# Kernel optimization log

Hardware: AMD Instinct MI355X
Metric: run time of the kernel (lower is better)

Reference implementation:

```python
import jax, jax.numpy as jnp
import numpy as np

# Model dims (match init_kwargs)
H = 1024            # hidden_size
I = 2048            # intermediate_size (per expert)
NH = 16             # num_heads
HD = H // NH        # head_dim = 64
E = 8               # num_experts
TOPK = 2
MAX_SEQ = 2048
EPS = 1e-6
NEG = -1e9


def precompute_freqs_cis(dim, max_seq_len, theta=10000.0):
    # Faithful to source: cat([cos, sin], dim=-1) -> shape [S, dim]
    pos = np.arange(max_seq_len, dtype=np.float32)
    freqs = np.arange(0, dim, 2, dtype=np.float32) / dim
    inv_freq = 1.0 / (theta ** freqs)
    f = np.einsum('i,j->ij', pos, inv_freq)
    return jnp.asarray(np.concatenate([np.cos(f), np.sin(f)], axis=-1), dtype=jnp.float32)


def setup_inputs() -> dict:
    key = jax.random.key(0)
    ks = jax.random.split(key, 12)
    B, S = 2, 1024
    s = lambda fan: 1.0 / np.sqrt(fan)
    inp = {
        'x': jax.random.normal(ks[0], (B, S, H), dtype=jnp.float32),
        'attn_norm_w': jnp.ones((H,), dtype=jnp.float32),
        'ffn_norm_w': jnp.ones((H,), dtype=jnp.float32),
        'wq': jax.random.normal(ks[1], (H, H), dtype=jnp.float32) * s(H),
        'wk': jax.random.normal(ks[2], (H, H), dtype=jnp.float32) * s(H),
        'wv': jax.random.normal(ks[3], (H, H), dtype=jnp.float32) * s(H),
        'wo': jax.random.normal(ks[4], (H, H), dtype=jnp.float32) * s(H),
        'router_w': jax.random.normal(ks[5], (H, E), dtype=jnp.float32) * s(H),
        'w1': jax.random.normal(ks[6], (E, H, I), dtype=jnp.float32) * s(H),
        'w3': jax.random.normal(ks[7], (E, H, I), dtype=jnp.float32) * s(H),
        'w2': jax.random.normal(ks[8], (E, I, H), dtype=jnp.float32) * s(I),
        'freqs_cis': precompute_freqs_cis(HD, MAX_SEQ),
    }
    return inp


def rmsnorm(x, w):
    rms = jnp.sqrt(jnp.mean(x * x, axis=-1, keepdims=True) + EPS)
    return w * (x / rms)


def apply_rope(x, freqs_cis):
    # x: [B, S, NH, HD]; faithful to source pairing (interleaved view of cat(cos,sin))
    B, S, nh, hd = x.shape
    xr = x.reshape(B, S, nh, hd // 2, 2)
    fr = freqs_cis[:S].reshape(1, S, 1, hd // 2, 2)  # position_ids = arange(S)
    a, b = xr[..., 0], xr[..., 1]
    cr, ci = fr[..., 0], fr[..., 1]
    out = jnp.stack([a * cr - b * ci, a * ci + b * cr], axis=-1)
    return out.reshape(B, S, nh, hd)


def attention(x, wq, wk, wv, wo, freqs_cis):
    B, S, _ = x.shape
    q = (x @ wq).reshape(B, S, NH, HD)
    k = (x @ wk).reshape(B, S, NH, HD)
    v = (x @ wv).reshape(B, S, NH, HD)
    q = apply_rope(q, freqs_cis)
    k = apply_rope(k, freqs_cis)
    # [B, NH, S, S]
    scores = jnp.einsum('bqhd,bkhd->bhqk', q, k) / np.sqrt(HD).astype(np.float32)
    causal = jnp.tril(jnp.ones((S, S), dtype=bool))
    scores = jnp.where(causal[None, None], scores, NEG)
    attn = jax.nn.softmax(scores, axis=-1)
    out = jnp.einsum('bhqk,bkhd->bqhd', attn, v).reshape(B, S, H)
    return out @ wo


def moe_ffn(x, router_w, w1, w2, w3):
    # x: [B, S, H] -> flatten tokens
    B, S, _ = x.shape
    xt = x.reshape(B * S, H)                      # [T, H]
    logits = xt @ router_w                        # [T, E]
    probs = jax.nn.softmax(logits, axis=-1)
    topv, topi = jax.lax.top_k(probs, TOPK)       # [T, K]
    topv = topv / jnp.sum(topv, axis=-1, keepdims=True)  # renormalize top-k weights
    # combine[t, e] = sum_k topv[t,k] * 1[topi[t,k]==e]
    combine = jnp.sum(topv[..., None] * jax.nn.one_hot(topi, E, dtype=xt.dtype), axis=1)  # [T, E]
    # SwiGLU experts, dense over experts (mathematically identical to no-drop routing)
    h1 = jnp.einsum('th,ehi->eti', xt, w1)
    h3 = jnp.einsum('th,ehi->eti', xt, w3)
    ye = jnp.einsum('eti,eih->eth', jax.nn.silu(h1) * h3, w2)  # [E, T, H]
    out = jnp.einsum('te,eth->th', combine, ye)
    return out.reshape(B, S, H)


def reference(x, attn_norm_w, ffn_norm_w, wq, wk, wv, wo, router_w, w1, w3, w2, freqs_cis):
    h = x + attention(rmsnorm(x, attn_norm_w), wq, wk, wv, wo, freqs_cis)
    out = h + moe_ffn(rmsnorm(h, ffn_norm_w), router_w, w1, w2, w3)
    return out
```

## Files before the change

### kernel.cpp

```cpp
#include <hip/hip_runtime.h>
#include <hip/hip_bf16.h>
#include <math.h>

#define HS 1024
#define IS 2048
#define NHEAD 16
#define HDIM 64
#define NEXP 8
#define BATCH 2
#define SEQ 1024
#define NTOK (BATCH*SEQ)
#define NASSIGN (NTOK*2)
#define QKVW 3072
#define PAD 72
#define MAXBLK 40

typedef short bf16x8 __attribute__((ext_vector_type(8)));
typedef float f32x4  __attribute__((ext_vector_type(4)));

__device__ __forceinline__ void ldsdma16(void* lds, const void* gp) {
    __builtin_amdgcn_global_load_lds(
        (const __attribute__((address_space(1))) void*)gp,
        (__attribute__((address_space(3))) void*)lds, 16, 0, 0);
}

__global__ void rmsnorm_split(const float* __restrict__ x, const float* __restrict__ w,
                              __hip_bfloat16* __restrict__ oh, __hip_bfloat16* __restrict__ ol) {
    int t = blockIdx.x;
    int tid = threadIdx.x;
    const float* row = x + (size_t)t * HS;
    float ss = 0.f;
    for (int i = tid; i < HS; i += 256) { float v = row[i]; ss += v * v; }
    for (int off = 32; off > 0; off >>= 1) ss += __shfl_down(ss, off);
    __shared__ float red[4];
    if ((tid & 63) == 0) red[tid >> 6] = ss;
    __syncthreads();
    float tot = red[0] + red[1] + red[2] + red[3];
    float rr = rsqrtf(tot / (float)HS + 1e-6f);
    for (int i = tid; i < HS; i += 256) {
        float v = w[i] * row[i] * rr;
        __hip_bfloat16 hi = __float2bfloat16(v);
        oh[(size_t)t * HS + i] = hi;
        ol[(size_t)t * HS + i] = __float2bfloat16(v - __bfloat162float(hi));
    }
}

__global__ void rmsnorm_dual(const float* __restrict__ x, const float* __restrict__ w,
                             float* __restrict__ outf, __hip_bfloat16* __restrict__ outb) {
    int t = blockIdx.x;
    int tid = threadIdx.x;
    const float* row = x + (size_t)t * HS;
    float ss = 0.f;
    for (int i = tid; i < HS; i += 256) { float v = row[i]; ss += v * v; }
    for (int off = 32; off > 0; off >>= 1) ss += __shfl_down(ss, off);
    __shared__ float red[4];
    if ((tid & 63) == 0) red[tid >> 6] = ss;
    __syncthreads();
    float tot = red[0] + red[1] + red[2] + red[3];
    float rr = rsqrtf(tot / (float)HS + 1e-6f);
    for (int i = tid; i < HS; i += 256) {
        float v = w[i] * row[i] * rr;
        outf[(size_t)t * HS + i] = v;
        outb[(size_t)t * HS + i] = __float2bfloat16(v);
    }
}

__global__ void transpose_split(const float* __restrict__ src,
                                __hip_bfloat16* __restrict__ dh, __hip_bfloat16* __restrict__ dl,
                                int R, int C, int rowOff) {
    __shared__ float tile[32][33];
    int c0 = blockIdx.x * 32, r0 = blockIdx.y * 32;
    int tx = threadIdx.x & 31, ty = threadIdx.x >> 5;
    #pragma unroll
    for (int i = 0; i < 4; i++) {
        int r = ty + i * 8;
        tile[r][tx] = src[(size_t)(r0 + r) * C + c0 + tx];
    }
    __syncthreads();
    #pragma unroll
    for (int i = 0; i < 4; i++) {
        int c = ty + i * 8;
        float v = tile[tx][c];
        __hip_bfloat16 hi = __float2bfloat16(v);
        size_t o = (size_t)(rowOff + c0 + c) * R + r0 + tx;
        dh[o] = hi;
        dl[o] = __float2bfloat16(v - __bfloat162float(hi));
    }
}

__global__ void transpose_bf16(const float* __restrict__ in, __hip_bfloat16* __restrict__ outp,
                               int R, int C) {
    __shared__ float tile[32][33];
    int e = blockIdx.z;
    const float* src = in + (size_t)e * R * C;
    __hip_bfloat16* dst = outp + (size_t)e * R * C;
    int c0 = blockIdx.x * 32, r0 = blockIdx.y * 32;
    int tx = threadIdx.x & 31, ty = threadIdx.x >> 5;
    #pragma unroll
    for (int i = 0; i < 4; i++) {
        int r = ty + i * 8;
        tile[r][tx] = src[(size_t)(r0 + r) * C + c0 + tx];
    }
    __syncthreads();
    #pragma unroll
    for (int i = 0; i < 4; i++) {
        int c = ty + i * 8;
        dst[(size_t)(c0 + c) * R + r0 + tx] = __float2bfloat16(tile[tx][c]);
    }
}

__global__ __launch_bounds__(256) void gemm_bf16x3(const __hip_bfloat16* __restrict__ Ah,
                                                   const __hip_bfloat16* __restrict__ Al,
                                                   const __hip_bfloat16* __restrict__ Bh,
                                                   const __hip_bfloat16* __restrict__ Bl,
                                                   const float* __restrict__ resid,
                                                   float* __restrict__ C,
                                                   int M, int N, int K) {
    __shared__ __align__(16) short Ahs[128][32];
    __shared__ __align__(16) short Als[128][32];
    __shared__ __align__(16) short Bhs[128][32];
    __shared__ __align__(16) short Bls[128][32];
    int bm = blockIdx.y * 128, bn = blockIdx.x * 128;
    int t = threadIdx.x;
    int wave = t >> 6, lane = t & 63;
    int wm = (wave & 1) * 64, wn = (wave >> 1) * 64;
    int fr = lane & 15, quad = lane >> 4;
    int r0 = wave * 32;
    int srow = lane >> 2;
    int schunk = (lane & 3) ^ ((lane >> 3) & 3);
    const __hip_bfloat16* pAh0 = Ah + (size_t)(bm + r0 + srow) * K + schunk * 8;
    const __hip_bfloat16* pAh1 = pAh0 + (size_t)16 * K;
    const __hip_bfloat16* pAl0 = Al + (size_t)(bm + r0 + srow) * K + schunk * 8;
    const __hip_bfloat16* pAl1 = pAl0 + (size_t)16 * K;
    const __hip_bfloat16* pBh0 = Bh + (size_t)(bn + r0 + srow) * K + schunk * 8;
    const __hip_bfloat16* pBh1 = pBh0 + (size_t)16 * K;
    const __hip_bfloat16* pBl0 = Bl + (size_t)(bn + r0 + srow) * K + schunk * 8;
    const __hip_bfloat16* pBl1 = pBl0 + (size_t)16 * K;
    int ca = (quad ^ ((fr >> 1) & 3)) * 8;

    f32x4 acc[4][4] = {};
    for (int k0 = 0; k0 < K; k0 += 32) {
        ldsdma16(&Ahs[r0][0],      pAh0 + k0);
        ldsdma16(&Ahs[r0 + 16][0], pAh1 + k0);
        ldsdma16(&Als[r0][0],      pAl0 + k0);
        ldsdma16(&Als[r0 + 16][0], pAl1 + k0);
        ldsdma16(&Bhs[r0][0],      pBh0 + k0);
        ldsdma16(&Bhs[r0 + 16][0], pBh1 + k0);
        ldsdma16(&Bls[r0][0],      pBl0 + k0);
        ldsdma16(&Bls[r0 + 16][0], pBl1 + k0);
        __syncthreads();
        bf16x8 ah[4], bh[4], x[4];
        #pragma unroll
        for (int i = 0; i < 4; i++) {
            ah[i] = *(const bf16x8*)&Ahs[wm + i * 16 + fr][ca];
            bh[i] = *(const bf16x8*)&Bhs[wn + i * 16 + fr][ca];
        }
        #pragma unroll
        for (int mi = 0; mi < 4; mi++)
            #pragma unroll
            for (int ni = 0; ni < 4; ni++)
                acc[mi][ni] = __builtin_amdgcn_mfma_f32_16x16x32_bf16(ah[mi], bh[ni], acc[mi][ni], 0, 0, 0);
        #pragma unroll
        for (int i = 0; i < 4; i++) x[i] = *(const bf16x8*)&Bls[wn + i * 16 + fr][ca];
        #pragma unroll
        for (int mi = 0; mi < 4; mi++)
            #pragma unroll
            for (int ni = 0; ni < 4; ni++)
                acc[mi][ni] = __builtin_amdgcn_mfma_f32_16x16x32_bf16(ah[mi], x[ni], acc[mi][ni], 0, 0, 0);
        #pragma unroll
        for (int i = 0; i < 4; i++) x[i] = *(const bf16x8*)&Als[wm + i * 16 + fr][ca];
        #pragma unroll
        for (int mi = 0; mi < 4; mi++)
            #pragma unroll
            for (int ni = 0; ni < 4; ni++)
                acc[mi][ni] = __builtin_amdgcn_mfma_f32_16x16x32_bf16(x[mi], bh[ni], acc[mi][ni], 0, 0, 0);
        __syncthreads();
    }
    int rq = quad * 4;
    #pragma unroll
    for (int mi = 0; mi < 4; mi++) {
        #pragma unroll
        for (int r = 0; r < 4; r++) {
            size_t rowo = (size_t)(bm + wm + mi * 16 + rq + r) * N + bn + wn;
            #pragma unroll
            for (int ni = 0; ni < 4; ni++) {
                float v = acc[mi][ni][r];
                size_t o = rowo + ni * 16 + fr;
                if (resid) v += resid[o];
                C[o] = v;
            }
        }
    }
}

__global__ void rope_convert(const float* __restrict__ qkv, const float* __restrict__ fc,
                             __hip_bfloat16* __restrict__ qh, __hip_bfloat16* __restrict__ ql,
                             __hip_bfloat16* __restrict__ kh, __hip_bfloat16* __restrict__ kl,
                             __hip_bfloat16* __restrict__ vh, __hip_bfloat16* __restrict__ vl) {
    int t = blockIdx.x;
    int s = t & (SEQ - 1);
    const float* row = qkv + (size_t)t * QKVW;
    size_t ob = (size_t)t * HS;
    for (int p = threadIdx.x; p < 512; p += 256) {
        int hh = p >> 5, j = p & 31;
        int col = hh * 64 + 2 * j;
        float cr = fc[s * HDIM + 2 * j];
        float ci = fc[s * HDIM + 2 * j + 1];
        float a = row[col], b = row[col + 1];
        float r0 = a * cr - b * ci, r1 = a * ci + b * cr;
        __hip_bfloat16 h0 = __float2bfloat16(r0), h1 = __float2bfloat16(r1);
        qh[ob + col] = h0;     ql[ob + col]     = __float2bfloat16(r0 - __bfloat162float(h0));
        qh[ob + col + 1] = h1; ql[ob + col + 1] = __float2bfloat16(r1 - __bfloat162float(h1));
        a = row[1024 + col]; b = row[1024 + col + 1];
        r0 = a * cr - b * ci; r1 = a * ci + b * cr;
        h0 = __float2bfloat16(r0); h1 = __float2bfloat16(r1);
        kh[ob + col] = h0;     kl[ob + col]     = __float2bfloat16(r0 - __bfloat162float(h0));
        kh[ob + col + 1] = h1; kl[ob + col + 1] = __float2bfloat16(r1 - __bfloat162float(h1));
        r0 = row[2048 + col]; r1 = row[2048 + col + 1];
        h0 = __float2bfloat16(r0); h1 = __float2bfloat16(r1);
        vh[ob + col] = h0;     vl[ob + col]     = __float2bfloat16(r0 - __bfloat162float(h0));
        vh[ob + col + 1] = h1; vl[ob + col + 1] = __float2bfloat16(r1 - __bfloat162float(h1));
    }
}

__global__ __launch_bounds__(256) void attn_partial(
        const __hip_bfloat16* __restrict__ qh, const __hip_bfloat16* __restrict__ ql,
        const __hip_bfloat16* __restrict__ kh, const __hip_bfloat16* __restrict__ kl,
        const __hip_bfloat16* __restrict__ vh, const __hip_bfloat16* __restrict__ vl,
        float* __restrict__ po, float* __restrict__ pm_g, float* __restrict__ pl_g) {
    int c = blockIdx.x, qt = blockIdx.y;
    int nc = (qt + 4) >> 2;
    if (c >= nc) return;
    int bh = blockIdx.z;
    int b = bh >> 4, h = bh & 15;
    int t0 = c * 4, t1 = min(t0 + 4, qt + 1);
    int tid = threadIdx.x;
    int wave = tid >> 6, lane = tid & 63;
    int fr = lane & 15, quad = lane >> 4;
    int w16 = wave * 16;
    __shared__ __align__(16) short Qh[64][PAD], Ql[64][PAD];
    __shared__ __align__(16) short KPh[64][PAD], KPl[64][PAD];
    __shared__ __align__(16) short Vhs[64][PAD], Vls[64][PAD];
    size_t hoff = (size_t)h * HDIM;
    int sr = tid >> 2, sg = tid & 3;
    {
        const __hip_bfloat16* qp  = qh + (size_t)(b * SEQ + qt * 64 + sr) * HS + hoff;
        const __hip_bfloat16* qp2 = ql + (size_t)(b * SEQ + qt * 64 + sr) * HS + hoff;
        *(uint4*)&Qh[sr][sg * 8]       = *(const uint4*)(qp + sg * 8);
        *(uint4*)&Qh[sr][(sg + 4) * 8] = *(const uint4*)(qp + (sg + 4) * 8);
        *(uint4*)&Ql[sr][sg * 8]       = *(const uint4*)(qp2 + sg * 8);
        *(uint4*)&Ql[sr][(sg + 4) * 8] = *(const uint4*)(qp2 + (sg + 4) * 8);
    }
    f32x4 o[4] = {};
    float mrow[4], lrow[4];
    #pragma unroll
    for (int i = 0; i < 4; i++) { mrow[i] = -1e30f; lrow[i] = 0.f; }
    int key0 = (tid & 31) * 2, ds = tid >> 5;
    __syncthreads();

    for (int kt = t0; kt < t1; kt++) {
        int kbase = kt * 64;
        {
            const __hip_bfloat16* kp  = kh + (size_t)(b * SEQ + kbase + sr) * HS + hoff;
            const __hip_bfloat16* kp2 = kl + (size_t)(b * SEQ + kbase + sr) * HS + hoff;
            *(uint4*)&KPh[sr][sg * 8]       = *(const uint4*)(kp + sg * 8);
            *(uint4*)&KPh[sr][(sg + 4) * 8] = *(const uint4*)(kp + (sg + 4) * 8);
            *(uint4*)&KPl[sr][sg * 8]       = *(const uint4*)(kp2 + sg * 8);
            *(uint4*)&KPl[sr][(sg + 4) * 8] = *(const uint4*)(kp2 + (sg + 4) * 8);
        }
        {
            const __hip_bfloat16* v0 = vh + (size_t)(b * SEQ + kbase + key0) * HS + hoff + ds * 8;
            uint4 A = *(const uint4*)v0;
            uint4 Bv = *(const uint4*)(v0 + HS);
            const unsigned short* ap = (const unsigned short*)&A;
            const unsigned short* bp = (const unsigned short*)&Bv;
            #pragma unroll
            for (int j = 0; j < 8; j++)
                *(unsigned*)&Vhs[ds * 8 + j][key0] = (unsigned)ap[j] | ((unsigned)bp[j] << 16);
            const __hip_bfloat16* v2 = vl + (size_t)(b * SEQ + kbase + key0) * HS + hoff + ds * 8;
            uint4 A2 = *(const uint4*)v2;
            uint4 B2 = *(const uint4*)(v2 + HS);
            const unsigned short* ap2 = (const unsigned short*)&A2;
            const unsigned short* bp2 = (const unsigned short*)&B2;
            #pragma unroll
            for (int j = 0; j < 8; j++)
                *(unsigned*)&Vls[ds * 8 + j][key0] = (unsigned)ap2[j] | ((unsigned)bp2[j] << 16);
        }
        __syncthreads();

        f32x4 s[4] = {};
        #pragma unroll
        for (int ks = 0; ks < 2; ks++) {
            bf16x8 a_h = *(const bf16x8*)&Qh[w16 + fr][quad * 8 + ks * 32];
            bf16x8 a_l = *(const bf16x8*)&Ql[w16 + fr][quad * 8 + ks * 32];
            #pragma unroll
            for (int ni = 0; ni < 4; ni++) {
                bf16x8 b_h = *(const bf16x8*)&KPh[ni * 16 + fr][quad * 8 + ks * 32];
                bf16x8 b_l = *(const bf16x8*)&KPl[ni * 16 + fr][quad * 8 + ks * 32];
                s[ni] = __builtin_amdgcn_mfma_f32_16x16x32_bf16(a_h, b_h, s[ni], 0, 0, 0);
                s[ni] = __builtin_amdgcn_mfma_f32_16x16x32_bf16(a_h, b_l, s[ni], 0, 0, 0);
                s[ni] = __builtin_amdgcn_mfma_f32_16x16x32_bf16(a_l, b_h, s[ni], 0, 0, 0);
            }
        }
        int qg = qt * 64 + w16 + quad * 4;
        #pragma unroll
        for (int ni = 0; ni < 4; ni++) {
            int kg = kbase + ni * 16 + fr;
            #pragma unroll
            for (int r = 0; r < 4; r++)
                s[ni][r] = (kg > qg + r) ? -1e9f : s[ni][r] * 0.125f;
        }
        #pragma unroll
        for (int r = 0; r < 4; r++) {
            float mx = fmaxf(fmaxf(s[0][r], s[1][r]), fmaxf(s[2][r], s[3][r]));
            #pragma unroll
            for (int wd = 1; wd < 16; wd <<= 1) mx = fmaxf(mx, __shfl_xor(mx, wd));
            float nm = fmaxf(mrow[r], mx);
            float alpha = __expf(mrow[r] - nm);
            float rs = 0.f;
            #pragma unroll
            for (int ni = 0; ni < 4; ni++) { float e = __expf(s[ni][r] - nm); s[ni][r] = e; rs += e; }
            #pragma unroll
            for (int wd = 1; wd < 16; wd <<= 1) rs += __shfl_xor(rs, wd);
            lrow[r] = lrow[r] * alpha + rs;
            mrow[r] = nm;
            o[0][r] *= alpha; o[1][r] *= alpha; o[2][r] *= alpha; o[3][r] *= alpha;
        }
        __syncthreads();
        #pragma unroll
        for (int ni = 0; ni < 4; ni++)
            #pragma unroll
            for (int r = 0; r < 4; r++) {
                float pv = s[ni][r];
                __hip_bfloat16 hi = __float2bfloat16(pv);
                __hip_bfloat16 lo = __float2bfloat16(pv - __bfloat162float(hi));
                KPh[w16 + quad * 4 + r][ni * 16 + fr] = *(short*)&hi;
                KPl[w16 + quad * 4 + r][ni * 16 + fr] = *(short*)&lo;
            }
        #pragma unroll
        for (int ks = 0; ks < 2; ks++) {
            bf16x8 p_h = *(const bf16x8*)&KPh[w16 + fr][quad * 8 + ks * 32];
            bf16x8 p_l = *(const bf16x8*)&KPl[w16 + fr][quad * 8 + ks * 32];
            #pragma unroll
            for (int ni = 0; ni < 4; ni++) {
                bf16x8 v_h = *(const bf16x8*)&Vhs[ni * 16 + fr][quad * 8 + ks * 32];
                bf16x8 v_l = *(const bf16x8*)&Vls[ni * 16 + fr][quad * 8 + ks * 32];
                o[ni] = __builtin_amdgcn_mfma_f32_16x16x32_bf16(p_h, v_h, o[ni], 0, 0, 0);
                o[ni] = __builtin_amdgcn_mfma_f32_16x16x32_bf16(p_h, v_l, o[ni], 0, 0, 0);
                o[ni] = __builtin_amdgcn_mfma_f32_16x16x32_bf16(p_l, v_h, o[ni], 0, 0, 0);
            }
        }
        __syncthreads();
    }
    int pidx = (bh * 16 + qt) * 4 + c;
    float* pob = po + (size_t)pidx * 4096;
    #pragma unroll
    for (int ni = 0; ni < 4; ni++)
        #pragma unroll
        for (int r = 0; r < 4; r++)
            pob[(w16 + quad * 4 + r) * 64 + ni * 16 + fr] = o[ni][r];
    if (fr == 0) {
        #pragma unroll
        for (int r = 0; r < 4; r++) {
            pm_g[pidx * 64 + w16 + quad * 4 + r] = mrow[r];
            pl_g[pidx * 64 + w16 + quad * 4 + r] = lrow[r];
        }
    }
}

__global__ void attn_merge(const float* __restrict__ po, const float* __restrict__ pm,
                           const float* __restrict__ pl,
                           __hip_bfloat16* __restrict__ ch, __hip_bfloat16* __restrict__ cl) {
    int qt = blockIdx.x, h = blockIdx.y, b = blockIdx.z;
    int bh = b * 16 + h;
    int nc = (qt + 4) >> 2;
    int base = (bh * 16 + qt) * 4;
    int tid = threadIdx.x;
    int r  = tid >> 2;
    int d0 = (tid & 3) * 16;
    float mstar = -1e30f;
    for (int c = 0; c < nc; c++) mstar = fmaxf(mstar, pm[(base + c) * 64 + r]);
    float a[4];
    float lsum = 0.f;
    for (int c = 0; c < nc; c++) {
        a[c] = __expf(pm[(base + c) * 64 + r] - mstar);
        lsum += a[c] * pl[(base + c) * 64 + r];
    }
    float inv = 1.f / lsum;
    size_t crow = (size_t)(b * SEQ + qt * 64 + r) * HS + h * HDIM;
    for (int dd = 0; dd < 16; dd += 4) {
        float4 acc = make_float4(0.f, 0.f, 0.f, 0.f);
        for (int c = 0; c < nc; c++) {
            float4 v = *(const float4*)(po + (size_t)(base + c) * 4096 + r * 64 + d0 + dd);
            acc.x += a[c] * v.x; acc.y += a[c] * v.y;
            acc.z += a[c] * v.z; acc.w += a[c] * v.w;
        }
        float vs[4] = {acc.x * inv, acc.y * inv, acc.z * inv, acc.w * inv};
        #pragma unroll
        for (int j = 0; j < 4; j++) {
            __hip_bfloat16 hi = __float2bfloat16(vs[j]);
            ch[crow + d0 + dd + j] = hi;
            cl[crow + d0 + dd + j] = __float2bfloat16(vs[j] - __bfloat162float(hi));
        }
    }
}

__global__ void router_kernel(const float* __restrict__ hn, const float* __restrict__ rw,
                              int* __restrict__ cnt, int* __restrict__ topEk,
                              float* __restrict__ topW) {
    int t = blockIdx.x;
    int lane = threadIdx.x;
    float acc[NEXP];
    #pragma unroll
    for (int e = 0; e < NEXP; e++) acc[e] = 0.f;
    const float* row = hn + (size_t)t * HS;
    for (int kk = lane; kk < HS; kk += 64) {
        float xv = row[kk];
        const float* r = rw + (size_t)kk * NEXP;
        #pragma unroll
        for (int e = 0; e < NEXP; e++) acc[e] += xv * r[e];
    }
    #pragma unroll
    for (int e = 0; e < NEXP; e++)
        for (int off = 32; off > 0; off >>= 1) acc[e] += __shfl_down(acc[e], off);
    if (lane == 0) {
        float mx = acc[0];
        #pragma unroll
        for (int e = 1; e < NEXP; e++) mx = fmaxf(mx, acc[e]);
        float p[NEXP]; float s = 0.f;
        #pragma unroll
        for (int e = 0; e < NEXP; e++) { p[e] = __expf(acc[e] - mx); s += p[e]; }
        int i0 = 0;
        #pragma unroll
        for (int e = 1; e < NEXP; e++) if (p[e] > p[i0]) i0 = e;
        int i1 = (i0 == 0) ? 1 : 0;
        #pragma unroll
        for (int e = 0; e < NEXP; e++) if (e != i0 && p[e] > p[i1]) i1 = e;
        float v0 = p[i0], v1 = p[i1], sn = v0 + v1;
        topEk[2 * t]     = i0; topW[2 * t]     = v0 / sn;
        topEk[2 * t + 1] = i1; topW[2 * t + 1] = v1 / sn;
        atomicAdd(&cnt[i0], 1);
        atomicAdd(&cnt[i1], 1);
    }
}

__global__ void offsets_kernel(const int* __restrict__ cnt, int* __restrict__ off,
                               int* __restrict__ blk_e, int* __restrict__ blk_r) {
    if (threadIdx.x == 0) {
        int o = 0, n = 0;
        for (int e = 0; e < NEXP; e++) {
            off[e] = o;
            for (int bm = 0; bm < cnt[e]; bm += 128) { blk_e[n] = e; blk_r[n] = bm; n++; }
            o += cnt[e];
        }
        for (; n < MAXBLK; n++) { blk_e[n] = -1; blk_r[n] = 0; }
    }
}

__global__ void scatter_kernel(const int* __restrict__ topEk, int* __restrict__ fill,
                               const int* __restrict__ off, const float* __restrict__ topW,
                               int* __restrict__ tok_list, float* __restrict__ wA) {
    int idx = blockIdx.x * 256 + threadIdx.x;
    int e = topEk[idx];
    int slot = atomicAdd(&fill[e], 1);
    int gidx = off[e] + slot;
    tok_list[gidx] = idx >> 1;
    wA[gidx] = topW[idx];
}

__global__ __launch_bounds__(256) void moe_up_mfma(const __hip_bfloat16* __restrict__ Abf,
                                                   const __hip_bfloat16* __restrict__ B1T,
                                                   const __hip_bfloat16* __restrict__ B3T,
                                                   __hip_bfloat16* __restrict__ g,
                                                   const int* __restrict__ cnt,
                                                   const int* __restrict__ off,
                                                   const int* __restrict__ tok_list,
                                                   const int* __restrict__ blk_e,
                                                   const int* __restrict__ blk_r) {
    int e = blk_e[blockIdx.y];
    if (e < 0) return;
    int bm = blk_r[blockIdx.y];
    int ce = cnt[e], oe = off[e];
    int bn = blockIdx.x * 128;
    const __hip_bfloat16* b1 = B1T + (size_t)e * IS * HS;
    const __hip_bfloat16* b3 = B3T + (size_t)e * IS * HS;

    __shared__ __align__(16) short As[128][32];
    __shared__ __align__(16) short B1s[128][32];
    __shared__ __align__(16) short B3s[128][32];

    int t = threadIdx.x;
    int wave = t >> 6, lane = t & 63;
    int wm = (wave & 1) * 64, wn = (wave >> 1) * 64;
    int fr = lane & 15, quad = lane >> 4;
    int r0 = wave * 32;
    int srow = lane >> 2;
    int schunk = (lane & 3) ^ ((lane >> 3) & 3);
    int tokA0 = tok_list[oe + min(bm + r0 + srow, ce - 1)];
    int tokA1 = tok_list[oe + min(bm + r0 + 16 + srow, ce - 1)];
    const __hip_bfloat16* pA0 = Abf + (size_t)tokA0 * HS + schunk * 8;
    const __hip_bfloat16* pA1 = Abf + (size_t)tokA1 * HS + schunk * 8;
    const __hip_bfloat16* pB1a = b1 + (size_t)(bn + r0 + srow) * HS + schunk * 8;
    const __hip_bfloat16* pB1b = pB1a + (size_t)16 * HS;
    const __hip_bfloat16* pB3a = b3 + (size_t)(bn + r0 + srow) * HS + schunk * 8;
    const __hip_bfloat16* pB3b = pB3a + (size_t)16 * HS;
    int ca = (quad ^ ((fr >> 1) & 3)) * 8;

    f32x4 acc1[4][4] = {};
    f32x4 acc3[4][4] = {};

    for (int k0 = 0; k0 < HS; k0 += 32) {
        ldsdma16(&As[r0][0],       pA0 + k0);
        ldsdma16(&As[r0 + 16][0],  pA1 + k0);
        ldsdma16(&B1s[r0][0],      pB1a + k0);
        ldsdma16(&B1s[r0 + 16][0], pB1b + k0);
        ldsdma16(&B3s[r0][0],      pB3a + k0);
        ldsdma16(&B3s[r0 + 16][0], pB3b + k0);
        __syncthreads();
        bf16x8 a[4], f1[4], f3[4];
        #pragma unroll
        for (int i = 0; i < 4; i++) {
            a[i]  = *(const bf16x8*)&As[wm + i * 16 + fr][ca];
            f1[i] = *(const bf16x8*)&B1s[wn + i * 16 + fr][ca];
            f3[i] = *(const bf16x8*)&B3s[wn + i * 16 + fr][ca];
        }
        #pragma unroll
        for (int mi = 0; mi < 4; mi++)
            #pragma unroll
            for (int ni = 0; ni < 4; ni++) {
                acc1[mi][ni] = __builtin_amdgcn_mfma_f32_16x16x32_bf16(a[mi], f1[ni], acc1[mi][ni], 0, 0, 0);
                acc3[mi][ni] = __builtin_amdgcn_mfma_f32_16x16x32_bf16(a[mi], f3[ni], acc3[mi][ni], 0, 0, 0);
            }
        __syncthreads();
    }
    int rq = quad * 4;
    #pragma unroll
    for (int mi = 0; mi < 4; mi++) {
        #pragma unroll
        for (int r = 0; r < 4; r++) {
            int slot = bm + wm + mi * 16 + rq + r;
            if (slot < ce) {
                size_t rowo = (size_t)(oe + slot) * IS + bn + wn;
                #pragma unroll
                for (int ni = 0; ni < 4; ni++) {
                    float x1 = acc1[mi][ni][r];
                    float x3 = acc3[mi][ni][r];
                    float sv = (x1 / (1.f + __expf(-x1))) * x3;
                    g[rowo + ni * 16 + fr] = __float2bfloat16(sv);
                }
            }
        }
    }
}

__global__ __launch_bounds__(256) void moe_down_mfma(const __hip_bfloat16* __restrict__ g,
                                                     const __hip_bfloat16* __restrict__ B2T,
                                                     float* __restrict__ out,
                                                     const int* __restrict__ cnt,
                                                     const int* __restrict__ off,
                                                     const int* __restrict__ tok_list,
                                                     const float* __restrict__ wA,
                                                     const int* __restrict__ blk_e,
                                                     const int* __restrict__ blk_r) {
    int e = blk_e[blockIdx.y];
    if (e < 0) return;
    int bm = blk_r[blockIdx.y];
    int ce = cnt[e], oe = off[e];
    int bn = blockIdx.x * 128;
    const __hip_bfloat16* b2 = B2T + (size_t)e * HS * IS;

    __shared__ __align__(16) short As[128][32];
    __shared__ __align__(16) short Bs[128][32];

    int t = threadIdx.x;
    int wave = t >> 6, lane = t & 63;
    int wm = (wave & 1) * 64, wn = (wave >> 1) * 64;
    int fr = lane & 15, quad = lane >> 4;
    int r0 = wave * 32;
    int srow = lane >> 2;
    int schunk = (lane & 3) ^ ((lane >> 3) & 3);
    int ga0 = oe + min(bm + r0 + srow, ce - 1);
    int ga1 = oe + min(bm + r0 + 16 + srow, ce - 1);
    const __hip_bfloat16* pA0 = g + (size_t)ga0 * IS + schunk * 8;
    const __hip_bfloat16* pA1 = g + (size_t)ga1 * IS + schunk * 8;
    const __hip_bfloat16* pBa = b2 + (size_t)(bn + r0 + srow) * IS + schunk * 8;
    const __hip_bfloat16* pBb = pBa + (size_t)16 * IS;
    int ca = (quad ^ ((fr >> 1) & 3)) * 8;

    f32x4 acc[4][4] = {};

    for (int k0 = 0; k0 < IS; k0 += 32) {
        ldsdma16(&As[r0][0],      pA0 + k0);
        ldsdma16(&As[r0 + 16][0], pA1 + k0);
        ldsdma16(&Bs[r0][0],      pBa + k0);
        ldsdma16(&Bs[r0 + 16][0], pBb + k0);
        __syncthreads();
        bf16x8 a[4], f[4];
        #pragma unroll
        for (int i = 0; i < 4; i++) {
            a[i] = *(const bf16x8*)&As[wm + i * 16 + fr][ca];
            f[i] = *(const bf16x8*)&Bs[wn + i * 16 + fr][ca];
        }
        #pragma unroll
        for (int mi = 0; mi < 4; mi++)
            #pragma unroll
            for (int ni = 0; ni < 4; ni++)
                acc[mi][ni] = __builtin_amdgcn_mfma_f32_16x16x32_bf16(a[mi], f[ni], acc[mi][ni], 0, 0, 0);
        __syncthreads();
    }
    int rq = quad * 4;
    #pragma unroll
    for (int mi = 0; mi < 4; mi++) {
        #pragma unroll
        for (int r = 0; r < 4; r++) {
            int slot = bm + wm + mi * 16 + rq + r;
            if (slot < ce) {
                int gidx = oe + slot;
                int tok = tok_list[gidx];
                float wgt = wA[gidx];
                size_t rowo = (size_t)tok * HS + bn + wn;
                #pragma unroll
                for (int ni = 0; ni < 4; ni++)
                    atomicAdd(out + rowo + ni * 16 + fr, wgt * acc[mi][ni][r]);
            }
        }
    }
}

extern "C" void kernel_launch(void* const* d_in, const int* in_sizes, int n_in,
                              void* d_out, int out_size, void* d_ws, size_t ws_size,
                              hipStream_t stream) {
    const float* x   = (const float*)d_in[0];
    const float* anw = (const float*)d_in[1];
    const float* fnw = (const float*)d_in[2];
    const float* wq  = (const float*)d_in[3];
    const float* wk  = (const float*)d_in[4];
    const float* wv  = (const float*)d_in[5];
    const float* wo  = (const float*)d_in[6];
    const float* rw  = (const float*)d_in[7];
    const float* w1  = (const float*)d_in[8];
    const float* w3  = (const float*)d_in[9];
    const float* w2  = (const float*)d_in[10];
    const float* fc  = (const float*)d_in[11];
    float* out = (float*)d_out;

    char* ws = (char*)d_ws;
    const size_t MB = 1024 * 1024;
    __hip_bfloat16* xn_h  = (__hip_bfloat16*)(ws + 0 * MB);
    __hip_bfloat16* xn_l  = (__hip_bfloat16*)(ws + 4 * MB);
    float*          qkv   = (float*)(ws + 8 * MB);
    __hip_bfloat16* WqT_h = (__hip_bfloat16*)(ws + 32 * MB);
    __hip_bfloat16* WqT_l = (__hip_bfloat16*)(ws + 38 * MB);
    __hip_bfloat16* woT_h = (__hip_bfloat16*)(ws + 44 * MB);
    __hip_bfloat16* woT_l = (__hip_bfloat16*)(ws + 46 * MB);
    float*          po    = (float*)(ws + 48 * MB);
    float*          pm    = (float*)(ws + 82 * MB);
    float*          plb   = (float*)(ws + 83 * MB);
    __hip_bfloat16* ctx_h = (__hip_bfloat16*)(ws + 84 * MB);
    __hip_bfloat16* ctx_l = (__hip_bfloat16*)(ws + 88 * MB);
    __hip_bfloat16* qhb   = (__hip_bfloat16*)(ws + 92 * MB);
    __hip_bfloat16* qlb   = (__hip_bfloat16*)(ws + 96 * MB);
    __hip_bfloat16* khb   = (__hip_bfloat16*)(ws + 100 * MB);
    __hip_bfloat16* klb   = (__hip_bfloat16*)(ws + 104 * MB);
    __hip_bfloat16* vhb   = (__hip_bfloat16*)(ws + 108 * MB);
    __hip_bfloat16* vlb   = (__hip_bfloat16*)(ws + 112 * MB);
    float*          hn    = (float*)(ws + 0 * MB);
    __hip_bfloat16* hn_bf = (__hip_bfloat16*)(ws + 8 * MB);
    __hip_bfloat16* w1T   = (__hip_bfloat16*)(ws + 12 * MB);
    __hip_bfloat16* w3T   = (__hip_bfloat16*)(ws + 44 * MB);
    __hip_bfloat16* w2T   = (__hip_bfloat16*)(ws + 76 * MB);
    __hip_bfloat16* gact  = (__hip_bfloat16*)(ws + 108 * MB);
    int* ibase    = (int*)(ws + 124 * MB);
    int* cnt      = ibase;
    int* fill     = ibase + 8;
    int* off      = ibase + 16;
    int* blk_e    = ibase + 24;
    int* blk_r    = ibase + 64;
    int* topEk    = ibase + 128;
    int* tok_list = ibase + 128 + NASSIGN;
    float* topW   = (float*)(ibase + 128 + 2 * NASSIGN);
    float* wA     = (float*)(ibase + 128 + 3 * NASSIGN);

    dim3 tg(HS / 32, HS / 32);
    transpose_split<<<tg, 256, 0, stream>>>(wq, WqT_h, WqT_l, HS, HS, 0);
    transpose_split<<<tg, 256, 0, stream>>>(wk, WqT_h, WqT_l, HS, HS, 1024);
    transpose_split<<<tg, 256, 0, stream>>>(wv, WqT_h, WqT_l, HS, HS, 2048);
    transpose_split<<<tg, 256, 0, stream>>>(wo, woT_h, woT_l, HS, HS, 0);
    rmsnorm_split<<<NTOK, 256, 0, stream>>>(x, anw, xn_h, xn_l);

    gemm_bf16x3<<<dim3(QKVW / 128, NTOK / 128), 256, 0, stream>>>(
        xn_h, xn_l, WqT_h, WqT_l, nullptr, qkv, NTOK, QKVW, HS);
    rope_convert<<<NTOK, 256, 0, stream>>>(qkv, fc, qhb, qlb, khb, klb, vhb, vlb);

    attn_partial<<<dim3(4, 16, 32), 256, 0, stream>>>(qhb, qlb, khb, klb, vhb, vlb, po, pm, plb);
    attn_merge<<<dim3(16, 16, 2), 256, 0, stream>>>(po, pm, plb, ctx_h, ctx_l);

    gemm_bf16x3<<<dim3(HS / 128, NTOK / 128), 256, 0, stream>>>(
        ctx_h, ctx_l, woT_h, woT_l, x, out, NTOK, HS, HS);

    rmsnorm_dual<<<NTOK, 256, 0, stream>>>(out, fnw, hn, hn_bf);
    transpose_bf16<<<dim3(IS / 32, HS / 32, NEXP), 256, 0, stream>>>(w1, w1T, HS, IS);
    transpose_bf16<<<dim3(IS / 32, HS / 32, NEXP), 256, 0, stream>>>(w3, w3T, HS, IS);
    transpose_bf16<<<dim3(HS / 32, IS / 32, NEXP), 256, 0, stream>>>(w2, w2T, IS, HS);

    hipMemsetAsync(cnt, 0, 16 * sizeof(int), stream);
    router_kernel<<<NTOK, 64, 0, stream>>>(hn, rw, cnt, topEk, topW);
    offsets_kernel<<<1, 64, 0, stream>>>(cnt, off, blk_e, blk_r);
    scatter_kernel<<<NASSIGN / 256, 256, 0, stream>>>(topEk, fill, off, topW, tok_list, wA);

    moe_up_mfma<<<dim3(IS / 128, MAXBLK), 256, 0, stream>>>(
        hn_bf, w1T, w3T, gact, cnt, off, tok_list, blk_e, blk_r);
    moe_down_mfma<<<dim3(HS / 128, MAXBLK), 256, 0, stream>>>(
        gact, w2T, out, cnt, off, tok_list, wA, blk_e, blk_r);
}
```

Baseline: 685.4 us.

## Double-buffer LDS tiles in the bf16x3 GEMM and MoE up/down kernels

```diff
diff --git a/kernel.cpp b/kernel.cpp
--- a/kernel.cpp
+++ b/kernel.cpp
@@ -116,10 +116,10 @@
                                                    const float* __restrict__ resid,
                                                    float* __restrict__ C,
                                                    int M, int N, int K) {
-    __shared__ __align__(16) short Ahs[128][32];
-    __shared__ __align__(16) short Als[128][32];
-    __shared__ __align__(16) short Bhs[128][32];
-    __shared__ __align__(16) short Bls[128][32];
+    __shared__ __align__(16) short Ahs[2][128][32];
+    __shared__ __align__(16) short Als[2][128][32];
+    __shared__ __align__(16) short Bhs[2][128][32];
+    __shared__ __align__(16) short Bls[2][128][32];
     int bm = blockIdx.y * 128, bn = blockIdx.x * 128;
     int t = threadIdx.x;
     int wave = t >> 6, lane = t & 63;
@@ -138,22 +138,37 @@
     const __hip_bfloat16* pBl1 = pBl0 + (size_t)16 * K;
     int ca = (quad ^ ((fr >> 1) & 3)) * 8;
 
+    ldsdma16(&Ahs[0][r0][0],      pAh0);
+    ldsdma16(&Ahs[0][r0 + 16][0], pAh1);
+    ldsdma16(&Als[0][r0][0],      pAl0);
+    ldsdma16(&Als[0][r0 + 16][0], pAl1);
+    ldsdma16(&Bhs[0][r0][0],      pBh0);
+    ldsdma16(&Bhs[0][r0 + 16][0], pBh1);
+    ldsdma16(&Bls[0][r0][0],      pBl0);
+    ldsdma16(&Bls[0][r0 + 16][0], pBl1);
+
     f32x4 acc[4][4] = {};
-    for (int k0 = 0; k0 < K; k0 += 32) {
-        ldsdma16(&Ahs[r0][0],      pAh0 + k0);
-        ldsdma16(&Ahs[r0 + 16][0], pAh1 + k0);
-        ldsdma16(&Als[r0][0],      pAl0 + k0);
-        ldsdma16(&Als[r0 + 16][0], pAl1 + k0);
-        ldsdma16(&Bhs[r0][0],      pBh0 + k0);
-        ldsdma16(&Bhs[r0 + 16][0], pBh1 + k0);
-        ldsdma16(&Bls[r0][0],      pBl0 + k0);
-        ldsdma16(&Bls[r0 + 16][0], pBl1 + k0);
+    int NIT = K >> 5;
+    for (int it = 0; it < NIT; it++) {
+        int cur = it & 1;
         __syncthreads();
+        if (it + 1 < NIT) {
+            int k1 = (it + 1) << 5;
+            int nxt = cur ^ 1;
+            ldsdma16(&Ahs[nxt][r0][0],      pAh0 + k1);
+            ldsdma16(&Ahs[nxt][r0 + 16][0], pAh1 + k1);
+            ldsdma16(&Als[nxt][r0][0],      pAl0 + k1);
+            ldsdma16(&Als[nxt][r0 + 16][0], pAl1 + k1);
+            ldsdma16(&Bhs[nxt][r0][0],      pBh0 + k1);
+            ldsdma16(&Bhs[nxt][r0 + 16][0], pBh1 + k1);
+            ldsdma16(&Bls[nxt][r0][0],      pBl0 + k1);
+            ldsdma16(&Bls[nxt][r0 + 16][0], pBl1 + k1);
+        }
         bf16x8 ah[4], bh[4], x[4];
         #pragma unroll
         for (int i = 0; i < 4; i++) {
-            ah[i] = *(const bf16x8*)&Ahs[wm + i * 16 + fr][ca];
-            bh[i] = *(const bf16x8*)&Bhs[wn + i * 16 + fr][ca];
+            ah[i] = *(const bf16x8*)&Ahs[cur][wm + i * 16 + fr][ca];
+            bh[i] = *(const bf16x8*)&Bhs[cur][wn + i * 16 + fr][ca];
         }
         #pragma unroll
         for (int mi = 0; mi < 4; mi++)
@@ -161,20 +176,19 @@
             for (int ni = 0; ni < 4; ni++)
                 acc[mi][ni] = __builtin_amdgcn_mfma_f32_16x16x32_bf16(ah[mi], bh[ni], acc[mi][ni], 0, 0, 0);
         #pragma unroll
-        for (int i = 0; i < 4; i++) x[i] = *(const bf16x8*)&Bls[wn + i * 16 + fr][ca];
+        for (int i = 0; i < 4; i++) x[i] = *(const bf16x8*)&Bls[cur][wn + i * 16 + fr][ca];
         #pragma unroll
         for (int mi = 0; mi < 4; mi++)
             #pragma unroll
             for (int ni = 0; ni < 4; ni++)
                 acc[mi][ni] = __builtin_amdgcn_mfma_f32_16x16x32_bf16(ah[mi], x[ni], acc[mi][ni], 0, 0, 0);
         #pragma unroll
-        for (int i = 0; i < 4; i++) x[i] = *(const bf16x8*)&Als[wm + i * 16 + fr][ca];
+        for (int i = 0; i < 4; i++) x[i] = *(const bf16x8*)&Als[cur][wm + i * 16 + fr][ca];
         #pragma unroll
         for (int mi = 0; mi < 4; mi++)
             #pragma unroll
             for (int ni = 0; ni < 4; ni++)
                 acc[mi][ni] = __builtin_amdgcn_mfma_f32_16x16x32_bf16(x[mi], bh[ni], acc[mi][ni], 0, 0, 0);
-        __syncthreads();
     }
     int rq = quad * 4;
     #pragma unroll
@@ -485,9 +499,9 @@
     const __hip_bfloat16* b1 = B1T + (size_t)e * IS * HS;
     const __hip_bfloat16* b3 = B3T + (size_t)e * IS * HS;
 
-    __shared__ __align__(16) short As[128][32];
-    __shared__ __align__(16) short B1s[128][32];
-    __shared__ __align__(16) short B3s[128][32];
+    __shared__ __align__(16) short As[2][128][32];
+    __shared__ __align__(16) short B1s[2][128][32];
+    __shared__ __align__(16) short B3s[2][128][32];
 
     int t = threadIdx.x;
     int wave = t >> 6, lane = t & 63;
@@ -506,23 +520,35 @@
     const __hip_bfloat16* pB3b = pB3a + (size_t)16 * HS;
     int ca = (quad ^ ((fr >> 1) & 3)) * 8;
 
+    ldsdma16(&As[0][r0][0],       pA0);
+    ldsdma16(&As[0][r0 + 16][0],  pA1);
+    ldsdma16(&B1s[0][r0][0],      pB1a);
+    ldsdma16(&B1s[0][r0 + 16][0], pB1b);
+    ldsdma16(&B3s[0][r0][0],      pB3a);
+    ldsdma16(&B3s[0][r0 + 16][0], pB3b);
+
     f32x4 acc1[4][4] = {};
     f32x4 acc3[4][4] = {};
-
-    for (int k0 = 0; k0 < HS; k0 += 32) {
-        ldsdma16(&As[r0][0],       pA0 + k0);
-        ldsdma16(&As[r0 + 16][0],  pA1 + k0);
-        ldsdma16(&B1s[r0][0],      pB1a + k0);
-        ldsdma16(&B1s[r0 + 16][0], pB1b + k0);
-        ldsdma16(&B3s[r0][0],      pB3a + k0);
-        ldsdma16(&B3s[r0 + 16][0], pB3b + k0);
+    const int NIT = HS >> 5;
+    for (int it = 0; it < NIT; it++) {
+        int cur = it & 1;
         __syncthreads();
+        if (it + 1 < NIT) {
+            int k1 = (it + 1) << 5;
+            int nxt = cur ^ 1;
+            ldsdma16(&As[nxt][r0][0],       pA0 + k1);
+            ldsdma16(&As[nxt][r0 + 16][0],  pA1 + k1);
+            ldsdma16(&B1s[nxt][r0][0],      pB1a + k1);
+            ldsdma16(&B1s[nxt][r0 + 16][0], pB1b + k1);
+            ldsdma16(&B3s[nxt][r0][0],      pB3a + k1);
+            ldsdma16(&B3s[nxt][r0 + 16][0], pB3b + k1);
+        }
         bf16x8 a[4], f1[4], f3[4];
         #pragma unroll
         for (int i = 0; i < 4; i++) {
-            a[i]  = *(const bf16x8*)&As[wm + i * 16 + fr][ca];
-            f1[i] = *(const bf16x8*)&B1s[wn + i * 16 + fr][ca];
-            f3[i] = *(const bf16x8*)&B3s[wn + i * 16 + fr][ca];
+            a[i]  = *(const bf16x8*)&As[cur][wm + i * 16 + fr][ca];
+            f1[i] = *(const bf16x8*)&B1s[cur][wn + i * 16 + fr][ca];
+            f3[i] = *(const bf16x8*)&B3s[cur][wn + i * 16 + fr][ca];
         }
         #pragma unroll
         for (int mi = 0; mi < 4; mi++)
@@ -531,7 +557,6 @@
                 acc1[mi][ni] = __builtin_amdgcn_mfma_f32_16x16x32_bf16(a[mi], f1[ni], acc1[mi][ni], 0, 0, 0);
                 acc3[mi][ni] = __builtin_amdgcn_mfma_f32_16x16x32_bf16(a[mi], f3[ni], acc3[mi][ni], 0, 0, 0);
             }
-        __syncthreads();
     }
     int rq = quad * 4;
     #pragma unroll
@@ -569,8 +594,8 @@
     int bn = blockIdx.x * 128;
     const __hip_bfloat16* b2 = B2T + (size_t)e * HS * IS;
 
-    __shared__ __align__(16) short As[128][32];
-    __shared__ __align__(16) short Bs[128][32];
+    __shared__ __align__(16) short As[2][128][32];
+    __shared__ __align__(16) short Bs[2][128][32];
 
     int t = threadIdx.x;
     int wave = t >> 6, lane = t & 63;
@@ -587,26 +612,35 @@
     const __hip_bfloat16* pBb = pBa + (size_t)16 * IS;
     int ca = (quad ^ ((fr >> 1) & 3)) * 8;
 
+    ldsdma16(&As[0][r0][0],      pA0);
+    ldsdma16(&As[0][r0 + 16][0], pA1);
+    ldsdma16(&Bs[0][r0][0],      pBa);
+    ldsdma16(&Bs[0][r0 + 16][0], pBb);
+
     f32x4 acc[4][4] = {};
-
-    for (int k0 = 0; k0 < IS; k0 += 32) {
-        ldsdma16(&As[r0][0],      pA0 + k0);
-        ldsdma16(&As[r0 + 16][0], pA1 + k0);
-        ldsdma16(&Bs[r0][0],      pBa + k0);
-        ldsdma16(&Bs[r0 + 16][0], pBb + k0);
+    const int NIT = IS >> 5;
+    for (int it = 0; it < NIT; it++) {
+        int cur = it & 1;
         __syncthreads();
+        if (it + 1 < NIT) {
+            int k1 = (it + 1) << 5;
+            int nxt = cur ^ 1;
+            ldsdma16(&As[nxt][r0][0],      pA0 + k1);
+            ldsdma16(&As[nxt][r0 + 16][0], pA1 + k1);
+            ldsdma16(&Bs[nxt][r0][0],      pBa + k1);
+            ldsdma16(&Bs[nxt][r0 + 16][0], pBb + k1);
+        }
         bf16x8 a[4], f[4];
         #pragma unroll
         for (int i = 0; i < 4; i++) {
-            a[i] = *(const bf16x8*)&As[wm + i * 16 + fr][ca];
-            f[i] = *(const bf16x8*)&Bs[wn + i * 16 + fr][ca];
+            a[i] = *(const bf16x8*)&As[cur][wm + i * 16 + fr][ca];
+            f[i] = *(const bf16x8*)&Bs[cur][wn + i * 16 + fr][ca];
         }
         #pragma unroll
         for (int mi = 0; mi < 4; mi++)
             #pragma unroll
             for (int ni = 0; ni < 4; ni++)
                 acc[mi][ni] = __builtin_amdgcn_mfma_f32_16x16x32_bf16(a[mi], f[ni], acc[mi][ni], 0, 0, 0);
-        __syncthreads();
     }
     int rq = quad * 4;
     #pragma unroll
```

New measurement: 671.4 us. -2.0%, faster.
